# Optimization experiments

Hardware: AMD Instinct MI355X
Metric: run time of the kernel (lower is better)

Reference implementation:

```python
import jax, jax.numpy as jnp
import numpy as np

EMBED = 2048
HIDDEN = 2048
T = 32768


def setup_inputs() -> dict:
    key = jax.random.key(0)
    k1, k2, k3, k4 = jax.random.split(key, 4)
    s_x = 1.0 / np.sqrt(EMBED)
    s_h = 1.0 / np.sqrt(HIDDEN)
    return {
        "X_embeddings": jax.random.normal(k1, (T, EMBED), dtype=jnp.float32),
        "Wx": jax.random.normal(k2, (EMBED, HIDDEN), dtype=jnp.float32) * s_x,
        "Wh": jax.random.normal(k3, (HIDDEN, HIDDEN), dtype=jnp.float32) * s_h,
        "b": jax.random.normal(k4, (HIDDEN,), dtype=jnp.float32) * 0.01,
    }


def reference(X_embeddings, Wx, Wh, b):
    # FastRecurrentRunner: H[0] = 0; for t in 0..T-2: H[t+1] = cell(X[t], H[t])
    # cell(x, h) = tanh(x @ Wx + h @ Wh + b)  (Elman RNN cell)
    dtype = X_embeddings.dtype
    # Precompute input projections for all steps at once (one big GEMM).
    xproj = X_embeddings[:-1] @ Wx + b  # [T-1, HIDDEN]

    def step(h, xp):
        h_next = jnp.tanh(xp + h @ Wh)
        return h_next, h_next

    h0 = jnp.zeros((HIDDEN,), dtype=dtype)
    _, H_tail = jax.lax.scan(step, h0, xproj)  # [T-1, HIDDEN]
    H = jnp.concatenate([h0[None, :], H_tail], axis=0)  # [T, HIDDEN]
    return H
```

## Files before the change

### kernel.cpp

```cpp
#include <hip/hip_runtime.h>
#include <math.h>

#define T_STEPS 32768
#define HID 2048
#define EMB 2048

#define BM 64
#define BN 64
#define BK 16

__global__ __launch_bounds__(256) void xproj_gemm(const float* __restrict__ X,
                                                  const float* __restrict__ Wx,
                                                  const float* __restrict__ bias,
                                                  float* __restrict__ XPout)
{
    __shared__ __align__(16) float As[BK][BM];
    __shared__ __align__(16) float Bs[BK][BN];

    const int tid = threadIdx.x;
    const int m0 = blockIdx.y * BM;
    const int n0 = blockIdx.x * BN;

    const int tn = tid & 15;
    const int tm = tid >> 4;
    const int am = tid >> 2;
    const int ak = (tid & 3) << 2;
    const int bk = tid >> 4;
    const int bn = (tid & 15) << 2;

    const int arow = m0 + am;
    const bool aval = arow < (T_STEPS - 1);

    float acc[4][4];
#pragma unroll
    for (int i = 0; i < 4; ++i)
#pragma unroll
        for (int j = 0; j < 4; ++j) acc[i][j] = 0.f;

    for (int k0 = 0; k0 < EMB; k0 += BK) {
        float4 av = make_float4(0.f, 0.f, 0.f, 0.f);
        if (aval) av = *(const float4*)&X[(size_t)arow * EMB + k0 + ak];
        float4 bv = *(const float4*)&Wx[(size_t)(k0 + bk) * HID + n0 + bn];

        __syncthreads();
        As[ak + 0][am] = av.x;
        As[ak + 1][am] = av.y;
        As[ak + 2][am] = av.z;
        As[ak + 3][am] = av.w;
        *(float4*)&Bs[bk][bn] = bv;
        __syncthreads();

#pragma unroll
        for (int k = 0; k < BK; ++k) {
            float4 a4 = *(const float4*)&As[k][tm << 2];
            float4 b4 = *(const float4*)&Bs[k][tn << 2];
            acc[0][0] += a4.x * b4.x; acc[0][1] += a4.x * b4.y;
            acc[0][2] += a4.x * b4.z; acc[0][3] += a4.x * b4.w;
            acc[1][0] += a4.y * b4.x; acc[1][1] += a4.y * b4.y;
            acc[1][2] += a4.y * b4.z; acc[1][3] += a4.y * b4.w;
            acc[2][0] += a4.z * b4.x; acc[2][1] += a4.z * b4.y;
            acc[2][2] += a4.z * b4.z; acc[2][3] += a4.z * b4.w;
            acc[3][0] += a4.w * b4.x; acc[3][1] += a4.w * b4.y;
            acc[3][2] += a4.w * b4.z; acc[3][3] += a4.w * b4.w;
        }
    }

    float4 bb = *(const float4*)&bias[n0 + (tn << 2)];
#pragma unroll
    for (int i = 0; i < 4; ++i) {
        int m = m0 + (tm << 2) + i;
        if (m < T_STEPS - 1) {
            float4 o;
            o.x = acc[i][0] + bb.x;
            o.y = acc[i][1] + bb.y;
            o.z = acc[i][2] + bb.z;
            o.w = acc[i][3] + bb.w;
            *(float4*)&XPout[(size_t)m * HID + n0 + (tn << 2)] = o;
        }
    }
}

typedef int v4i __attribute__((ext_vector_type(4)));
typedef int v2i __attribute__((ext_vector_type(2)));

__device__ __forceinline__ float dot4(float4 a, float4 b)
{
    return a.x * b.x + a.y * b.y + a.z * b.z + a.w * b.w;
}

__device__ __forceinline__ void poll4_sc0(const void* p, v4i& a, v4i& b, v4i& c, v4i& d)
{
    asm volatile("global_load_dwordx4 %0, %4, off sc0\n\t"
                 "global_load_dwordx4 %1, %4, off offset:16 sc0\n\t"
                 "global_load_dwordx4 %2, %4, off offset:32 sc0\n\t"
                 "global_load_dwordx4 %3, %4, off offset:48 sc0\n\t"
                 "s_waitcnt vmcnt(0)"
                 : "=&v"(a), "=&v"(b), "=&v"(c), "=&v"(d) : "v"(p) : "memory");
}
__device__ __forceinline__ void poll4_sys(const void* p, v4i& a, v4i& b, v4i& c, v4i& d)
{
    asm volatile("global_load_dwordx4 %0, %4, off sc0 sc1\n\t"
                 "global_load_dwordx4 %1, %4, off offset:16 sc0 sc1\n\t"
                 "global_load_dwordx4 %2, %4, off offset:32 sc0 sc1\n\t"
                 "global_load_dwordx4 %3, %4, off offset:48 sc0 sc1\n\t"
                 "s_waitcnt vmcnt(0)"
                 : "=&v"(a), "=&v"(b), "=&v"(c), "=&v"(d) : "v"(p) : "memory");
}
__device__ __forceinline__ void st8_sc0(void* p, v2i v)
{
    asm volatile("global_store_dwordx2 %0, %1, off sc0" :: "v"(p), "v"(v) : "memory");
}
__device__ __forceinline__ void st8_sys(void* p, v2i v)
{
    asm volatile("global_store_dwordx2 %0, %1, off sc0 sc1" :: "v"(p), "v"(v) : "memory");
}

__device__ __forceinline__ unsigned short bf16rne(float f)
{
    unsigned u = __float_as_uint(f);
    u += 0x7fffu + ((u >> 16) & 1u);
    return (unsigned short)(u >> 16);
}
__device__ __forceinline__ float bfup(unsigned short s)
{
    return __uint_as_float((unsigned)s << 16);
}

__global__ __launch_bounds__(256, 1) void rnn_scan_fast(const float* __restrict__ Wh,
                                                        const float* __restrict__ XP,
                                                        float* __restrict__ H,
                                                        unsigned long long* __restrict__ hcomm)
{
    __shared__ __align__(16) ushort4 Wl2b[128][64];
    __shared__ __align__(16) float hlds[2][HID];
    __shared__ float pacc[4][64];

    const int tid = threadIdx.x;
    const int wave = tid >> 6;
    const int lane = tid & 63;
    const int g = blockIdx.x & 7;
    const int rank = blockIdx.x >> 3;
    const int bc0 = rank * 64;
    unsigned long long* hcg = hcomm + (size_t)g * (2 * HID);

    float4 wreg[96];
    {
        const float* wp = Wh + (size_t)(384 * wave) * HID + bc0 + lane;
#pragma unroll
        for (int i = 0; i < 96; ++i) {
            wreg[i].x = wp[(size_t)(4 * i + 0) * HID];
            wreg[i].y = wp[(size_t)(4 * i + 1) * HID];
            wreg[i].z = wp[(size_t)(4 * i + 2) * HID];
            wreg[i].w = wp[(size_t)(3 + 4 * i) * HID];
        }
    }
    for (int k = 0; k < 32; ++k) {
        int id = k * 256 + tid;
        int r4 = id >> 6, c = id & 63;
        const float* p = Wh + (size_t)(1536 + 4 * r4) * HID + bc0 + c;
        ushort4 u;
        u.x = bf16rne(p[0]);
        u.y = bf16rne(p[(size_t)HID]);
        u.z = bf16rne(p[2 * (size_t)HID]);
        u.w = bf16rne(p[3 * (size_t)HID]);
        Wl2b[r4][c] = u;
    }
    __syncthreads();

    for (int t = 0; t < T_STEPS - 1; ++t) {
        const int par = t & 1;

        float xpv = 0.f;
        if (wave == 0) xpv = XP[(size_t)t * HID + bc0 + lane];

        const char* pb = (const char*)hcg + (((size_t)par * HID + 8 * (size_t)tid) << 3);
        v4i e0, e1, e2, e3;
        int round = 0;
        for (;;) {
            if ((round & 15) == 15) poll4_sys(pb, e0, e1, e2, e3);
            else                    poll4_sc0(pb, e0, e1, e2, e3);
            if (((e0.y ^ t) | (e0.w ^ t) | (e1.y ^ t) | (e1.w ^ t) |
                 (e2.y ^ t) | (e2.w ^ t) | (e3.y ^ t) | (e3.w ^ t)) == 0) break;
            ++round;
        }

        v4i h0; h0.x = e0.x; h0.y = e0.z; h0.z = e1.x; h0.w = e1.z;
        v4i h1; h1.x = e2.x; h1.y = e2.z; h1.z = e3.x; h1.w = e3.z;
        *(v4i*)&hlds[par][8 * tid] = h0;
        *(v4i*)&hlds[par][8 * tid + 4] = h1;
        __syncthreads();

        const float* hb = hlds[par];
        const float* hbr = &hb[384 * wave];
        float a0 = 0.f, a1 = 0.f, a2 = 0.f, a3 = 0.f;
#pragma unroll
        for (int i = 0; i < 96; i += 4) {
            a0 += dot4(wreg[i],     *(const float4*)&hbr[4 * i]);
            a1 += dot4(wreg[i + 1], *(const float4*)&hbr[4 * i + 4]);
            a2 += dot4(wreg[i + 2], *(const float4*)&hbr[4 * i + 8]);
            a3 += dot4(wreg[i + 3], *(const float4*)&hbr[4 * i + 12]);
        }
        float b0 = 0.f, b1 = 0.f;
#pragma unroll
        for (int j = 0; j < 32; j += 2) {
            const int r4 = 32 * wave + j;
            ushort4 ua = Wl2b[r4][lane];
            ushort4 ub = Wl2b[r4 + 1][lane];
            float4 qa = *(const float4*)&hb[1536 + 4 * r4];
            float4 qb = *(const float4*)&hb[1536 + 4 * r4 + 4];
            b0 += bfup(ua.x) * qa.x + bfup(ua.y) * qa.y
                + bfup(ua.z) * qa.z + bfup(ua.w) * qa.w;
            b1 += bfup(ub.x) * qb.x + bfup(ub.y) * qb.y
                + bfup(ub.z) * qb.z + bfup(ub.w) * qb.w;
        }
        pacc[wave][lane] = ((a0 + a1) + (a2 + a3)) + (b0 + b1);
        __syncthreads();

        if (wave == 0) {
            float tot = pacc[0][lane] + pacc[1][lane] + pacc[2][lane] + pacc[3][lane];
            float hv = tanhf(xpv + tot);
            v2i e; e.x = __float_as_int(hv); e.y = t + 1;
            char* pa = (char*)hcg + (((size_t)(par ^ 1) * HID + bc0 + lane) << 3);
            st8_sc0(pa, e);
            st8_sys(pa, e);
            if (g == 0) H[(size_t)(t + 1) * HID + bc0 + lane] = hv;
        }
    }
}

#define NBLK_R3 64
#define TPB_R3 1024
#define CPB_R3 32
#define CPW_R3 2

__device__ __forceinline__ v4i uncached_load16(const void* p)
{
    v4i r;
    asm volatile("global_load_dwordx4 %0, %1, off sc0 sc1\n\t"
                 "s_waitcnt vmcnt(0)"
                 : "=v"(r) : "v"(p) : "memory");
    return r;
}
__device__ __forceinline__ void uncached_store16(void* p, v4i v)
{
    asm volatile("global_store_dwordx4 %0, %1, off sc0 sc1"
                 :: "v"(p), "v"(v) : "memory");
}

__global__ __launch_bounds__(TPB_R3, 4) void rnn_scan_r3(const float* __restrict__ Wh,
                                                         float* __restrict__ H,
                                                         unsigned long long* __restrict__ hcomm)
{
    __shared__ __align__(16) float hlds[2][HID];
    __shared__ float pad[18432];

    const int tid = threadIdx.x;
    const int wave = tid >> 6;
    const int lane = tid & 63;
    const int c0 = blockIdx.x * CPB_R3 + wave * CPW_R3;

    if ((((size_t)hcomm) >> 22) & 1) ((volatile float*)pad)[tid] = 0.f;

    float4 w0[8], w1[8];
#pragma unroll
    for (int k = 0; k < 8; ++k) {
        const int r = 4 * lane + 256 * k;
        const float* p = Wh + (size_t)r * HID + c0;
        w0[k].x = p[0];                     w1[k].x = p[1];
        w0[k].y = p[(size_t)HID];           w1[k].y = p[(size_t)HID + 1];
        w0[k].z = p[(size_t)(2 * HID)];     w1[k].z = p[(size_t)(2 * HID) + 1];
        w0[k].w = p[(size_t)(3 * HID)];     w1[k].w = p[(size_t)(3 * HID) + 1];
    }

    for (int t = 0; t < T_STEPS - 1; ++t) {
        float2 xp = make_float2(0.f, 0.f);
        if (lane == 0) xp = *(const float2*)&H[(size_t)(t + 1) * HID + c0];

        const char* slot = (const char*)hcomm +
                           (((size_t)(t & 1) * HID + 2 * (size_t)tid) << 3);
        v4i e;
        do {
            e = uncached_load16(slot);
        } while (e.y != t || e.w != t);

        *(float2*)&hlds[t & 1][2 * tid] =
            make_float2(__int_as_float(e.x), __int_as_float(e.z));
        __syncthreads();

        const float* hb = hlds[t & 1];
        float s0 = 0.f, s1 = 0.f;
#pragma unroll
        for (int k = 0; k < 8; ++k) {
            float4 hh = *(const float4*)&hb[4 * lane + 256 * k];
            s0 += hh.x * w0[k].x + hh.y * w0[k].y + hh.z * w0[k].z + hh.w * w0[k].w;
            s1 += hh.x * w1[k].x + hh.y * w1[k].y + hh.z * w1[k].z + hh.w * w1[k].w;
        }
#pragma unroll
        for (int m = 1; m < 64; m <<= 1) {
            s0 += __shfl_xor(s0, m, 64);
            s1 += __shfl_xor(s1, m, 64);
        }

        if (lane == 0) {
            float h0 = tanhf(xp.x + s0);
            float h1 = tanhf(xp.y + s1);
            v4i pub;
            pub.x = __float_as_int(h0); pub.y = t + 1;
            pub.z = __float_as_int(h1); pub.w = t + 1;
            uncached_store16((char*)hcomm +
                             (((size_t)((t + 1) & 1) * HID + (size_t)c0) << 3), pub);
            *(float2*)&H[(size_t)(t + 1) * HID + c0] = make_float2(h0, h1);
        }
    }
}

static void launch_r3_path(const float* X, const float* Wx, const float* Wh,
                           const float* b, float* H, void* d_ws, hipStream_t stream)
{
    unsigned long long* hcomm = (unsigned long long*)d_ws;
    hipMemsetAsync(H, 0, HID * sizeof(float), stream);
    hipMemsetAsync(d_ws, 0, 2 * HID * sizeof(unsigned long long), stream);

    dim3 ggrid(HID / BN, T_STEPS / BM);
    xproj_gemm<<<ggrid, 256, 0, stream>>>(X, Wx, b, H + HID);

    const float* whp = Wh; float* hp = H; unsigned long long* cp = hcomm;
    void* args[] = { (void*)&whp, (void*)&hp, (void*)&cp };
    hipLaunchCooperativeKernel((const void*)rnn_scan_r3, dim3(NBLK_R3),
                               dim3(TPB_R3), args, 0, stream);
}

extern "C" void kernel_launch(void* const* d_in, const int* in_sizes, int n_in,
                              void* d_out, int out_size, void* d_ws, size_t ws_size,
                              hipStream_t stream)
{
    const float* X  = (const float*)d_in[0];
    const float* Wx = (const float*)d_in[1];
    const float* Wh = (const float*)d_in[2];
    const float* b  = (const float*)d_in[3];
    float* H = (float*)d_out;

    const size_t XP_BYTES = (size_t)(T_STEPS - 1) * HID * sizeof(float);
    const size_t XP_OFF   = 512 * 1024;
    const bool big_ws = ws_size >= XP_OFF + XP_BYTES;

    int nb = 0;
    bool fast_ok = big_ws &&
        (hipOccupancyMaxActiveBlocksPerMultiprocessor(&nb, (const void*)rnn_scan_fast,
                                                      256, 0) == hipSuccess) && nb >= 1;

    if (fast_ok) {
        unsigned long long* hcomm = (unsigned long long*)d_ws;
        float* XPb = (float*)((char*)d_ws + XP_OFF);

        hipMemsetAsync(H, 0, HID * sizeof(float), stream);
        hipMemsetAsync(d_ws, 0, 8 * 2 * HID * sizeof(unsigned long long), stream);

        dim3 ggrid(HID / BN, T_STEPS / BM);
        xproj_gemm<<<ggrid, 256, 0, stream>>>(X, Wx, b, XPb);

        const float* whp = Wh; const float* xpp = XPb;
        float* hp = H; unsigned long long* cp = hcomm;
        void* args[] = { (void*)&whp, (void*)&xpp, (void*)&hp, (void*)&cp };
        hipError_t err = hipLaunchCooperativeKernel((const void*)rnn_scan_fast,
                                                    dim3(256), dim3(256), args, 0, stream);
        if (err != hipSuccess) {
            launch_r3_path(X, Wx, Wh, b, H, d_ws, stream);
        }
    } else {
        launch_r3_path(X, Wx, Wh, b, H, d_ws, stream);
    }
}
```

Before: 141.8 ms.

## Double scan block size to eight waves and rebalance register/LDS weight split

Raises the recurrent scan kernel from 256 to 512 threads per block. Each wave now owns 256 rows of the Wh column slice: 176 rows stay in fp32 registers and 80 rows sit in LDS as bf16. Polling now has each thread load half as many flag/value pairs, and the final reduction sums eight partial results instead of four. The aim is to shorten the per-step dot product and polling latency by spreading the work over more waves, at the cost of a wider block barrier, and the store order of the sys/sc0 flag writes is swapped.

```diff
diff --git a/kernel.cpp b/kernel.cpp
--- a/kernel.cpp
+++ b/kernel.cpp
@@ -88,23 +88,19 @@
     return a.x * b.x + a.y * b.y + a.z * b.z + a.w * b.w;
 }
 
-__device__ __forceinline__ void poll4_sc0(const void* p, v4i& a, v4i& b, v4i& c, v4i& d)
-{
-    asm volatile("global_load_dwordx4 %0, %4, off sc0\n\t"
-                 "global_load_dwordx4 %1, %4, off offset:16 sc0\n\t"
-                 "global_load_dwordx4 %2, %4, off offset:32 sc0\n\t"
-                 "global_load_dwordx4 %3, %4, off offset:48 sc0\n\t"
+__device__ __forceinline__ void poll2_sc0(const void* p, v4i& a, v4i& b)
+{
+    asm volatile("global_load_dwordx4 %0, %2, off sc0\n\t"
+                 "global_load_dwordx4 %1, %2, off offset:16 sc0\n\t"
                  "s_waitcnt vmcnt(0)"
-                 : "=&v"(a), "=&v"(b), "=&v"(c), "=&v"(d) : "v"(p) : "memory");
-}
-__device__ __forceinline__ void poll4_sys(const void* p, v4i& a, v4i& b, v4i& c, v4i& d)
-{
-    asm volatile("global_load_dwordx4 %0, %4, off sc0 sc1\n\t"
-                 "global_load_dwordx4 %1, %4, off offset:16 sc0 sc1\n\t"
-                 "global_load_dwordx4 %2, %4, off offset:32 sc0 sc1\n\t"
-                 "global_load_dwordx4 %3, %4, off offset:48 sc0 sc1\n\t"
+                 : "=&v"(a), "=&v"(b) : "v"(p) : "memory");
+}
+__device__ __forceinline__ void poll2_sys(const void* p, v4i& a, v4i& b)
+{
+    asm volatile("global_load_dwordx4 %0, %2, off sc0 sc1\n\t"
+                 "global_load_dwordx4 %1, %2, off offset:16 sc0 sc1\n\t"
                  "s_waitcnt vmcnt(0)"
-                 : "=&v"(a), "=&v"(b), "=&v"(c), "=&v"(d) : "v"(p) : "memory");
+                 : "=&v"(a), "=&v"(b) : "v"(p) : "memory");
 }
 __device__ __forceinline__ void st8_sc0(void* p, v2i v)
 {
@@ -126,14 +122,16 @@
     return __uint_as_float((unsigned)s << 16);
 }
 
-__global__ __launch_bounds__(256, 1) void rnn_scan_fast(const float* __restrict__ Wh,
-                                                        const float* __restrict__ XP,
-                                                        float* __restrict__ H,
-                                                        unsigned long long* __restrict__ hcomm)
-{
-    __shared__ __align__(16) ushort4 Wl2b[128][64];
+#define SCAN_TPB 512
+
+__global__ __launch_bounds__(SCAN_TPB, 2) void rnn_scan_fast(const float* __restrict__ Wh,
+                                                             const float* __restrict__ XP,
+                                                             float* __restrict__ H,
+                                                             unsigned long long* __restrict__ hcomm)
+{
+    __shared__ __align__(16) ushort4 Wb[8][20][64];
     __shared__ __align__(16) float hlds[2][HID];
-    __shared__ float pacc[4][64];
+    __shared__ float pacc[8][64];
 
     const int tid = threadIdx.x;
     const int wave = tid >> 6;
@@ -143,27 +141,25 @@
     const int bc0 = rank * 64;
     unsigned long long* hcg = hcomm + (size_t)g * (2 * HID);
 
-    float4 wreg[96];
+    float4 wreg[44];
     {
-        const float* wp = Wh + (size_t)(384 * wave) * HID + bc0 + lane;
-#pragma unroll
-        for (int i = 0; i < 96; ++i) {
+        const float* wp = Wh + (size_t)(256 * wave) * HID + bc0 + lane;
+#pragma unroll
+        for (int i = 0; i < 44; ++i) {
             wreg[i].x = wp[(size_t)(4 * i + 0) * HID];
             wreg[i].y = wp[(size_t)(4 * i + 1) * HID];
             wreg[i].z = wp[(size_t)(4 * i + 2) * HID];
-            wreg[i].w = wp[(size_t)(3 + 4 * i) * HID];
-        }
-    }
-    for (int k = 0; k < 32; ++k) {
-        int id = k * 256 + tid;
-        int r4 = id >> 6, c = id & 63;
-        const float* p = Wh + (size_t)(1536 + 4 * r4) * HID + bc0 + c;
+            wreg[i].w = wp[(size_t)(4 * i + 3) * HID];
+        }
+    }
+    for (int j = 0; j < 20; ++j) {
+        const float* p = Wh + (size_t)(256 * wave + 176 + 4 * j) * HID + bc0 + lane;
         ushort4 u;
         u.x = bf16rne(p[0]);
         u.y = bf16rne(p[(size_t)HID]);
         u.z = bf16rne(p[2 * (size_t)HID]);
         u.w = bf16rne(p[3 * (size_t)HID]);
-        Wl2b[r4][c] = u;
+        Wb[wave][j][lane] = u;
     }
     __syncthreads();
 
@@ -173,57 +169,47 @@
         float xpv = 0.f;
         if (wave == 0) xpv = XP[(size_t)t * HID + bc0 + lane];
 
-        const char* pb = (const char*)hcg + (((size_t)par * HID + 8 * (size_t)tid) << 3);
-        v4i e0, e1, e2, e3;
+        const char* pb = (const char*)hcg + (((size_t)par * HID + 4 * (size_t)tid) << 3);
+        v4i e0, e1;
         int round = 0;
         for (;;) {
-            if ((round & 15) == 15) poll4_sys(pb, e0, e1, e2, e3);
-            else                    poll4_sc0(pb, e0, e1, e2, e3);
-            if (((e0.y ^ t) | (e0.w ^ t) | (e1.y ^ t) | (e1.w ^ t) |
-                 (e2.y ^ t) | (e2.w ^ t) | (e3.y ^ t) | (e3.w ^ t)) == 0) break;
+            if ((round & 15) == 15) poll2_sys(pb, e0, e1);
+            else                    poll2_sc0(pb, e0, e1);
+            if (((e0.y ^ t) | (e0.w ^ t) | (e1.y ^ t) | (e1.w ^ t)) == 0) break;
             ++round;
         }
 
-        v4i h0; h0.x = e0.x; h0.y = e0.z; h0.z = e1.x; h0.w = e1.z;
-        v4i h1; h1.x = e2.x; h1.y = e2.z; h1.z = e3.x; h1.w = e3.z;
-        *(v4i*)&hlds[par][8 * tid] = h0;
-        *(v4i*)&hlds[par][8 * tid + 4] = h1;
-        __syncthreads();
-
-        const float* hb = hlds[par];
-        const float* hbr = &hb[384 * wave];
-        float a0 = 0.f, a1 = 0.f, a2 = 0.f, a3 = 0.f;
-#pragma unroll
-        for (int i = 0; i < 96; i += 4) {
-            a0 += dot4(wreg[i],     *(const float4*)&hbr[4 * i]);
-            a1 += dot4(wreg[i + 1], *(const float4*)&hbr[4 * i + 4]);
-            a2 += dot4(wreg[i + 2], *(const float4*)&hbr[4 * i + 8]);
-            a3 += dot4(wreg[i + 3], *(const float4*)&hbr[4 * i + 12]);
-        }
-        float b0 = 0.f, b1 = 0.f;
-#pragma unroll
-        for (int j = 0; j < 32; j += 2) {
-            const int r4 = 32 * wave + j;
-            ushort4 ua = Wl2b[r4][lane];
-            ushort4 ub = Wl2b[r4 + 1][lane];
-            float4 qa = *(const float4*)&hb[1536 + 4 * r4];
-            float4 qb = *(const float4*)&hb[1536 + 4 * r4 + 4];
-            b0 += bfup(ua.x) * qa.x + bfup(ua.y) * qa.y
-                + bfup(ua.z) * qa.z + bfup(ua.w) * qa.w;
-            b1 += bfup(ub.x) * qb.x + bfup(ub.y) * qb.y
-                + bfup(ub.z) * qb.z + bfup(ub.w) * qb.w;
-        }
-        pacc[wave][lane] = ((a0 + a1) + (a2 + a3)) + (b0 + b1);
+        v4i hv; hv.x = e0.x; hv.y = e0.z; hv.z = e1.x; hv.w = e1.z;
+        *(v4i*)&hlds[par][4 * tid] = hv;
+        __syncthreads();
+
+        const float* hb = &hlds[par][256 * wave];
+        float a0 = 0.f, a1 = 0.f;
+#pragma unroll
+        for (int i = 0; i < 44; i += 2) {
+            a0 += dot4(wreg[i],     *(const float4*)&hb[4 * i]);
+            a1 += dot4(wreg[i + 1], *(const float4*)&hb[4 * i + 4]);
+        }
+        float b0 = 0.f;
+#pragma unroll
+        for (int j = 0; j < 20; ++j) {
+            ushort4 u = Wb[wave][j][lane];
+            float4 q = *(const float4*)&hb[176 + 4 * j];
+            b0 += bfup(u.x) * q.x + bfup(u.y) * q.y
+                + bfup(u.z) * q.z + bfup(u.w) * q.w;
+        }
+        pacc[wave][lane] = (a0 + a1) + b0;
         __syncthreads();
 
         if (wave == 0) {
-            float tot = pacc[0][lane] + pacc[1][lane] + pacc[2][lane] + pacc[3][lane];
-            float hv = tanhf(xpv + tot);
-            v2i e; e.x = __float_as_int(hv); e.y = t + 1;
+            float tot = ((pacc[0][lane] + pacc[1][lane]) + (pacc[2][lane] + pacc[3][lane]))
+                      + ((pacc[4][lane] + pacc[5][lane]) + (pacc[6][lane] + pacc[7][lane]));
+            float hvn = tanhf(xpv + tot);
+            v2i e; e.x = __float_as_int(hvn); e.y = t + 1;
             char* pa = (char*)hcg + (((size_t)(par ^ 1) * HID + bc0 + lane) << 3);
+            st8_sys(pa, e);
             st8_sc0(pa, e);
-            st8_sys(pa, e);
-            if (g == 0) H[(size_t)(t + 1) * HID + bc0 + lane] = hv;
+            if (g == 0) H[(size_t)(t + 1) * HID + bc0 + lane] = hvn;
         }
     }
 }
@@ -347,7 +333,7 @@
     int nb = 0;
     bool fast_ok = big_ws &&
         (hipOccupancyMaxActiveBlocksPerMultiprocessor(&nb, (const void*)rnn_scan_fast,
-                                                      256, 0) == hipSuccess) && nb >= 1;
+                                                      SCAN_TPB, 0) == hipSuccess) && nb >= 1;
 
     if (fast_ok) {
         unsigned long long* hcomm = (unsigned long long*)d_ws;
@@ -363,7 +349,7 @@
         float* hp = H; unsigned long long* cp = hcomm;
         void* args[] = { (void*)&whp, (void*)&xpp, (void*)&hp, (void*)&cp };
         hipError_t err = hipLaunchCooperativeKernel((const void*)rnn_scan_fast,
-                                                    dim3(256), dim3(256), args, 0, stream);
+                                                    dim3(256), dim3(SCAN_TPB), args, 0, stream);
         if (err != hipSuccess) {
             launch_r3_path(X, Wx, Wh, b, H, d_ws, stream);
         }
```

Measured after the change: 135.2 ms. 1.05x faster.
